# Performance work log

Hardware: AMD Instinct MI355X
Metric: run time of the kernel (lower is better)

## Reference

```python
import jax, jax.numpy as jnp
import numpy as np

NUM_CLASSES = 7
CLASS_WEIGHT = 1.0
BOX_WEIGHT = 1.0


def _linear_sum_assignment(cost):
    """Exact Hungarian via shortest augmenting paths (Jonker-Volgenant style).
    Matches scipy.optimize.linear_sum_assignment for rectangular matrices:
    returns (row_ind, col_ind) of length min(n, m), row_ind sorted ascending."""
    C = np.asarray(cost, dtype=np.float64)
    transposed = C.shape[0] > C.shape[1]
    if transposed:
        C = C.T
    n, m = C.shape  # n <= m
    u = np.zeros(n + 1)
    v = np.zeros(m + 1)
    p = np.zeros(m + 1, dtype=np.int64)    # p[j]: row matched to col j (1-based); 0 = free
    way = np.zeros(m + 1, dtype=np.int64)
    for i in range(1, n + 1):
        p[0] = i
        j0 = 0
        minv = np.full(m + 1, np.inf)
        used = np.zeros(m + 1, dtype=bool)
        while True:
            used[j0] = True
            i0 = p[j0]
            cur = C[i0 - 1] - u[i0] - v[1:]
            free = ~used[1:]
            better = free & (cur < minv[1:])
            minv[1:][better] = cur[better]
            way[1:][better] = j0
            masked = np.where(free, minv[1:], np.inf)
            j0n = int(np.argmin(masked)) + 1
            delta = masked[j0n - 1]
            uj = np.nonzero(used)[0]
            u[p[uj]] += delta
            v[uj] -= delta
            minv[1:][free] -= delta
            j0 = j0n
            if p[j0] == 0:
                break
        while j0 != 0:   # augment along alternating path
            j1 = way[j0]
            p[j0] = p[j1]
            j0 = j1
    cols = np.nonzero(p[1:] > 0)[0]
    rows = p[1:][cols] - 1
    if transposed:
        rows, cols = cols, rows
    order = np.argsort(rows)
    return rows[order], cols[order]


def _cost_matrices(pred_logits, pred_boxes, gt_labels, gt_boxes):
    """Batched cost: class_weight * (-log_softmax gathered at gt labels) + box_weight * L1 cdist on xyz."""
    B, Q, _ = pred_logits.shape
    M = gt_labels.shape[1]
    log_probs = jax.nn.log_softmax(pred_logits, axis=-1)                       # (B,Q,C)
    idx = jnp.broadcast_to(gt_labels[:, None, :], (B, Q, M))
    class_cost = -jnp.take_along_axis(log_probs, idx, axis=2)                  # (B,Q,M)
    box_cost = jnp.sum(jnp.abs(pred_boxes[:, :, None, :3] - gt_boxes[:, None, :, :3]), axis=-1)  # (B,Q,M)
    return CLASS_WEIGHT * class_cost + BOX_WEIGHT * box_cost


def _matched_loss(pred_logits, pred_boxes, gt_labels, gt_boxes, rows, cols):
    B = pred_logits.shape[0]
    bidx = jnp.arange(B)[:, None]
    ml = pred_logits[bidx, rows]          # (B,M,C) matched logits
    mb = pred_boxes[bidx, rows]           # (B,M,7) matched boxes
    gl = gt_labels[bidx, cols]            # (B,M)
    gb = gt_boxes[bidx, cols]             # (B,M,7)
    logp = jax.nn.log_softmax(ml, axis=-1)
    ce = -jnp.mean(jnp.take_along_axis(logp, gl[..., None], axis=-1)[..., 0], axis=1)  # (B,)
    l1 = jnp.mean(jnp.abs(mb - gb), axis=(1, 2))                                       # (B,)
    return jnp.mean(CLASS_WEIGHT * ce + BOX_WEIGHT * l1)


def setup_inputs() -> dict:
    key = jax.random.key(0)
    k1, k2, k3, k4 = jax.random.split(key, 4)
    B, Q, M = 128, 900, 100
    return {
        'pred_logits': jax.random.normal(k1, (B, Q, NUM_CLASSES), dtype=jnp.float32),
        'pred_boxes': jax.random.normal(k2, (B, Q, 7), dtype=jnp.float32),
        'gt_labels': jax.random.randint(k3, (B, M), 0, NUM_CLASSES, dtype=jnp.int32),
        'gt_boxes': jax.random.normal(k4, (B, M, 7), dtype=jnp.float32),
    }


def reference(pred_logits, pred_boxes, gt_labels, gt_boxes):
    B = pred_logits.shape[0]
    M = gt_labels.shape[1]
    # Assignment is done on detached costs (host-side), matching the original module.
    cost = np.asarray(_cost_matrices(pred_logits, pred_boxes, gt_labels, gt_boxes))
    rows = np.zeros((B, M), dtype=np.int64)
    cols = np.zeros((B, M), dtype=np.int64)
    for b in range(B):
        r, c = _linear_sum_assignment(cost[b])
        rows[b], cols[b] = r, c
    return _matched_loss(pred_logits, pred_boxes, gt_labels, gt_boxes,
                         jnp.asarray(rows), jnp.asarray(cols))
```

## Files before the change

### kernel.cpp

```cpp
#include <hip/hip_runtime.h>
#include <math.h>


#define NQ   900
#define NG   100
#define NC   7
#define CPL  15
#define ROUNDS 10
#define INFF __builtin_inff()

__device__ __forceinline__ float readlane_f(float x, int l) {
  return __int_as_float(__builtin_amdgcn_readlane(__float_as_int(x), l));
}

template<int CTRL>
__device__ __forceinline__ void dpp_amin_step(float &v, int &ix) {
  float v2 = __int_as_float(__builtin_amdgcn_update_dpp(
      __float_as_int(v), __float_as_int(v), CTRL, 0xf, 0xf, false));
  int i2 = __builtin_amdgcn_update_dpp(ix, ix, CTRL, 0xf, 0xf, false);
  ix = (v2 < v) ? i2 : ix;
  v  = fminf(v, v2);
}
__device__ __forceinline__ void wave_amin_b(float v, int ix, float &ov, int &oi) {
  dpp_amin_step<0x111>(v, ix);
  dpp_amin_step<0x112>(v, ix);
  dpp_amin_step<0x114>(v, ix);
  dpp_amin_step<0x118>(v, ix);
  dpp_amin_step<0x142>(v, ix);
  dpp_amin_step<0x143>(v, ix);
  ov = readlane_f(v, 63);
  oi = __builtin_amdgcn_readlane(ix, 63);
}

template<int CTRL>
__device__ __forceinline__ void dpp_amin2_step(float &a, int &ia, float &b, int &ib) {
  const int INFI = 0x7f800000;
  float a2 = __int_as_float(__builtin_amdgcn_update_dpp(
      INFI, __float_as_int(a), CTRL, 0xf, 0xf, false));
  float b2 = __int_as_float(__builtin_amdgcn_update_dpp(
      INFI, __float_as_int(b), CTRL, 0xf, 0xf, false));
  int ia2 = __builtin_amdgcn_update_dpp(0, ia, CTRL, 0xf, 0xf, false);
  int ib2 = __builtin_amdgcn_update_dpp(0, ib, CTRL, 0xf, 0xf, false);
  bool sw = a2 < a;
  float hi = sw ? a  : a2;  int ihi = sw ? ia  : ia2;
  float lo = sw ? a2 : a;   int ilo = sw ? ia2 : ia;
  bool t1 = b2 < b;
  float bb = t1 ? b2 : b;   int ibb = t1 ? ib2 : ib;
  bool t2 = hi < bb;
  b = t2 ? hi : bb;         ib = t2 ? ihi : ibb;
  a = lo; ia = ilo;
}
__device__ __forceinline__ void wave_amin2_b(float a, int ia, float b, int ib,
    float &o1, int &oc1, float &o2, int &oc2) {
  dpp_amin2_step<0x111>(a, ia, b, ib);
  dpp_amin2_step<0x112>(a, ia, b, ib);
  dpp_amin2_step<0x114>(a, ia, b, ib);
  dpp_amin2_step<0x118>(a, ia, b, ib);
  dpp_amin2_step<0x142>(a, ia, b, ib);
  dpp_amin2_step<0x143>(a, ia, b, ib);
  o1 = readlane_f(a, 63); oc1 = __builtin_amdgcn_readlane(ia, 63);
  o2 = readlane_f(b, 63); oc2 = __builtin_amdgcn_readlane(ib, 63);
}

template<int CTRL>
__device__ __forceinline__ float dpp_add_step(float x) {
  int y = __builtin_amdgcn_update_dpp(0, __float_as_int(x),
                                      CTRL, 0xf, 0xf, true);
  return x + __int_as_float(y);
}
__device__ __forceinline__ float wave_sum_b(float x) {
  x = dpp_add_step<0x111>(x);
  x = dpp_add_step<0x112>(x);
  x = dpp_add_step<0x114>(x);
  x = dpp_add_step<0x118>(x);
  x = dpp_add_step<0x142>(x);
  x = dpp_add_step<0x143>(x);
  return __int_as_float(__builtin_amdgcn_readlane(__float_as_int(x), 63));
}
__device__ __forceinline__ void gl_lds16(const float* g, float* lds_base) {
  __builtin_amdgcn_global_load_lds(
      (const __attribute__((address_space(1))) unsigned int*)g,
      (__attribute__((address_space(3))) unsigned int*)lds_base, 16, 0, 0);
}
__device__ __forceinline__ float sel7v(float a0,float a1,float a2,float a3,
                                       float a4,float a5,float a6,int lab){
  float r = a0;
  r = lab==1 ? a1 : r;  r = lab==2 ? a2 : r;  r = lab==3 ? a3 : r;
  r = lab==4 ? a4 : r;  r = lab==5 ? a5 : r;  r = lab==6 ? a6 : r;
  return r;
}

__global__ __launch_bounds__(256, 1) void hungarian_fused_kernel(
    const float* __restrict__ logits, const float* __restrict__ pboxes,
    const int* __restrict__ glabels, const float* __restrict__ gboxes,
    float* __restrict__ out, float inv_B)
{
  const int b = blockIdx.x, tid = threadIdx.x;
  const int lane = tid & 63, w = tid >> 6;

  __shared__ __align__(16) float s_raw[NQ * NC];
  __shared__ __align__(16) float s_nlpT[NC * 1024];
  __shared__ __align__(16) float s_pb[960 * NC];
  __shared__ __align__(16) float s_gb[NG * NC];
  __shared__ __align__(16) int   s_glab[NG];
  __shared__ float s_u[NG + 1];
  __shared__ float s_v[CPL * 64];
  __shared__ int   s_p[NQ];
  __shared__ unsigned s_bid[NQ];
  __shared__ int   s_rmatch[NG];
  __shared__ float s_bm1[NG], s_bm2[NG];
  __shared__ int   s_bc[NG];
  __shared__ unsigned long long s_fm[2];
  __shared__ float s_f1v[NG]; __shared__ int s_f1c[NG];
  __shared__ float s_f2v[NG]; __shared__ int s_f2c[NG];
  __shared__ int   s_mlist[128];

  {
    const float* Lg = logits + (size_t)b * NQ * NC;
    const float* Pg = pboxes + (size_t)b * NQ * NC;
    const float* Gg = gboxes + (size_t)b * NG * NC;
    const int*   Bg = glabels + (size_t)b * NG;
    #pragma unroll
    for (int t = 0; t < 7; t++) {
      int i = (t << 8) + tid;
      if (i < (NQ * NC) / 4) {
        gl_lds16(Lg + i * 4, s_raw + ((t << 8) + (w << 6)) * 4);
        gl_lds16(Pg + i * 4, s_pb  + ((t << 8) + (w << 6)) * 4);
      }
    }
    if (tid < (NG * NC) / 4) gl_lds16(Gg + tid * 4, s_gb + (w << 6) * 4);
    if (tid < NG / 4) gl_lds16((const float*)Bg + tid * 4, (float*)s_glab);
    for (int i = tid; i < (960 - NQ) * NC; i += 256) s_pb[NQ * NC + i] = 0.f;
    for (int c = tid; c < NQ; c += 256) { s_p[c] = 0x7fffffff; s_bid[c] = 0xFFFFFFFFu; }
    for (int i = tid; i < CPL * 64; i += 256) s_v[i] = 0.f;
    if (tid == 0) s_u[0] = 0.f;
  }
  __syncthreads();

  for (int i = tid; i < 960; i += 256) {
    int L = i & 63, t = i >> 6;
    int q = L * CPL + t;
    float o[NC];
    if (q < NQ) {
      float x[NC];
      #pragma unroll
      for (int c = 0; c < NC; c++) x[c] = s_raw[q * NC + c];
      float mx = x[0];
      #pragma unroll
      for (int c = 1; c < NC; c++) mx = fmaxf(mx, x[c]);
      float tt[NC]; float se = 0.f;
      #pragma unroll
      for (int c = 0; c < NC; c++) { tt[c] = x[c] - mx; se += __expf(tt[c]); }
      float lg = __logf(se);
      #pragma unroll
      for (int c = 0; c < NC; c++) o[c] = lg - tt[c];
    } else {
      #pragma unroll
      for (int c = 0; c < NC; c++) o[c] = INFF;
    }
    #pragma unroll
    for (int c = 0; c < NC; c++) s_nlpT[c * 1024 + t * 64 + L] = o[c];
  }
  __syncthreads();

  const bool lval = (lane < NQ / CPL);
  float cpx[CPL], cpy[CPL], cpz[CPL];
  #pragma unroll
  for (int t = 0; t < CPL; t++) {
    int c = lane * CPL + t;
    cpx[t]=s_pb[c*NC+0]; cpy[t]=s_pb[c*NC+1]; cpz[t]=s_pb[c*NC+2];
  }

  for (int rl = 0; rl < 25; rl++) {
    int r = w * 25 + rl;
    int lab = s_glab[r];
    float gx = s_gb[r*NC+0], gy = s_gb[r*NC+1], gz = s_gb[r*NC+2];
    float m1 = INFF; int c1t = 0;
    #pragma unroll
    for (int t = 0; t < CPL; t++) {
      float nl = s_nlpT[lab*1024 + t*64 + lane];
      float bs = fabsf(cpx[t]-gx)+fabsf(cpy[t]-gy)+fabsf(cpz[t]-gz);
      float cost = nl + bs;
      bool lt1 = cost < m1;
      c1t = lt1 ? t : c1t;
      m1 = fminf(m1, cost);
    }
    float w1; int col;
    wave_amin_b(m1, lane * CPL + c1t, w1, col);
    if (lane == 0) {
      s_u[r + 1] = w1;
      s_bc[r] = col;
      atomicMin(&s_p[col], r + 1);
    }
  }
  __syncthreads();
  for (int c = tid; c < NQ; c += 256) if (s_p[c] == 0x7fffffff) s_p[c] = 0;
  if (tid < NG) {
    int c = s_bc[tid];
    s_rmatch[tid] = (s_p[c] == tid + 1) ? c + 1 : 0;
  }
  __syncthreads();

  for (int round = 0; round < ROUNDS; round++) {
    if (w == 0) {
      unsigned long long m = __ballot(s_rmatch[lane] == 0);
      if (lane == 0) s_fm[0] = m;
    } else if (w == 1) {
      unsigned long long m = __ballot((lane < NG - 64) && s_rmatch[64 + lane] == 0);
      if (lane == 0) s_fm[1] = m;
    }
    __syncthreads();
    const unsigned long long fm0r = s_fm[0], fm1r = s_fm[1];
    if ((fm0r | fm1r) == 0) break;
    float vreg[CPL];
    #pragma unroll
    for (int t = 0; t < CPL; t++) vreg[t] = s_v[t*64 + lane];
    {
      unsigned long long mm0 = fm0r, mm1 = fm1r;
      int idx = 0;
      while (mm0 | mm1) {
        int r;
        if (mm0) { int b2 = (int)__builtin_ctzll(mm0); mm0 &= mm0 - 1; r = b2; }
        else     { int b2 = (int)__builtin_ctzll(mm1); mm1 &= mm1 - 1; r = 64 + b2; }
        if ((idx++ & 3) != w) continue;
        int lab = s_glab[r];
        float gx = s_gb[r*NC+0], gy = s_gb[r*NC+1], gz = s_gb[r*NC+2];
        float m1 = INFF, m2 = INFF; int c1t = 0;
        #pragma unroll
        for (int t = 0; t < CPL; t++) {
          float nl = s_nlpT[lab*1024 + t*64 + lane];
          float bs = fabsf(cpx[t]-gx)+fabsf(cpy[t]-gy)+fabsf(cpz[t]-gz);
          float cost = (nl + bs) - vreg[t];
          bool lt1 = cost < m1;
          m2 = lt1 ? m1 : fminf(m2, cost);
          c1t = lt1 ? t : c1t;
          m1 = fminf(m1, cost);
        }
        float w1, w2; int col1, dumc;
        wave_amin2_b(m1, lane * CPL + c1t, m2, 0, w1, col1, w2, dumc);
        if (lane == 0) {
          s_bm1[r] = w1; s_bm2[r] = w2; s_bc[r] = col1;
          atomicMin(&s_bid[col1],
                    (__float_as_uint(w1) & 0xFFFFFF80u) | (unsigned)(r + 1));
        }
      }
    }
    __syncthreads();
    if (tid < NG) {
      bool wasfree = (tid < 64) ? ((fm0r >> tid) & 1ull)
                                : ((fm1r >> (tid - 64)) & 1ull);
      if (wasfree) {
        int c = s_bc[tid];
        if ((s_bid[c] & 0x7Fu) == (unsigned)(tid + 1)) {
          int dold = s_p[c];
          s_p[c] = tid + 1;
          s_rmatch[tid] = c + 1;
          if (dold > 0) s_rmatch[dold - 1] = 0;
          s_u[tid + 1] = s_bm2[tid];
          s_v[(c % CPL) * 64 + (c / CPL)] -= (s_bm2[tid] - s_bm1[tid]);
        }
      }
    }
    __syncthreads();
    if (tid < NG) {
      bool wasfree = (tid < 64) ? ((fm0r >> tid) & 1ull)
                                : ((fm1r >> (tid - 64)) & 1ull);
      if (wasfree) s_bid[s_bc[tid]] = 0xFFFFFFFFu;
    }
  }
  __syncthreads();

  if (w == 0) {
    unsigned long long m = __ballot(s_rmatch[lane] == 0);
    if (lane == 0) s_fm[0] = m;
  } else if (w == 1) {
    unsigned long long m = __ballot((lane < NG - 64) && s_rmatch[64 + lane] == 0);
    if (lane == 0) s_fm[1] = m;
  }
  __syncthreads();
  const unsigned long long ff0 = s_fm[0], ff1 = s_fm[1];
  const int nfinal = __popcll(ff0) + __popcll(ff1);

  if (nfinal > 0) {
    float vreg[CPL];
    #pragma unroll
    for (int t = 0; t < CPL; t++) vreg[t] = s_v[t*64 + lane];
    unsigned long long mm0 = ff0, mm1 = ff1;
    int idx = 0;
    while (mm0 | mm1) {
      int r;
      if (mm0) { int b2 = (int)__builtin_ctzll(mm0); mm0 &= mm0 - 1; r = b2; }
      else     { int b2 = (int)__builtin_ctzll(mm1); mm1 &= mm1 - 1; r = 64 + b2; }
      if ((idx++ & 3) != w) continue;
      int lab = s_glab[r];
      float gx = s_gb[r*NC+0], gy = s_gb[r*NC+1], gz = s_gb[r*NC+2];
      float m1 = INFF; int c1t = 0;
      #pragma unroll
      for (int t = 0; t < CPL; t++) {
        float nl = s_nlpT[lab*1024 + t*64 + lane];
        float bs = fabsf(cpx[t]-gx)+fabsf(cpy[t]-gy)+fabsf(cpz[t]-gz);
        float cost = (nl + bs) - vreg[t];
        bool lt1 = cost < m1;
        c1t = lt1 ? t : c1t;
        m1 = fminf(m1, cost);
      }
      float w1; int col;
      wave_amin_b(m1, lane * CPL + c1t, w1, col);
      if (lane == 0) { s_u[r + 1] = w1; s_bc[r] = col; }
    }
    __syncthreads();
    if (tid < NG) {
      bool wasfree = (tid < 64) ? ((ff0 >> tid) & 1ull)
                                : ((ff1 >> (tid - 64)) & 1ull);
      if (wasfree) {
        int c = s_bc[tid];
        if (s_p[c] == 0) atomicMin(&s_bid[c], (unsigned)tid);
      }
    }
    __syncthreads();
    if (tid < NG) {
      bool wasfree = (tid < 64) ? ((ff0 >> tid) & 1ull)
                                : ((ff1 >> (tid - 64)) & 1ull);
      if (wasfree) {
        int c = s_bc[tid];
        if (s_p[c] == 0 && s_bid[c] == (unsigned)tid) {
          s_p[c] = tid + 1;
          s_rmatch[tid] = c + 1;
        }
      }
    }
    __syncthreads();
    if (w == 0) {
      unsigned long long m = __ballot(s_rmatch[lane] == 0);
      if (lane == 0) s_fm[0] = m;
    } else if (w == 1) {
      unsigned long long m = __ballot((lane < NG - 64) && s_rmatch[64 + lane] == 0);
      if (lane == 0) s_fm[1] = m;
    }
    __syncthreads();
  }

  const unsigned long long gg0 = s_fm[0], gg1 = s_fm[1];
  const int nf2 = __popcll(gg0) + __popcll(gg1);

  if (nf2 > 0) {
  unsigned fmask = 0;
  if (lval) {
    #pragma unroll
    for (int t = 0; t < CPL; t++)
      if (s_p[lane * CPL + t] == 0) fmask |= (1u << t);
  }

  auto top2row = [&](int lab, float gx, float gy, float gz,
                     float &o1v, int &o1c, float &o2v, int &o2c) {
    float m1 = INFF, m2 = INFF; int c1 = 0, c2 = 0;
    #pragma unroll
    for (int t = 0; t < CPL; t++) {
      float nl = s_nlpT[lab*1024 + t*64 + lane];
      float bs = fabsf(cpx[t]-gx)+fabsf(cpy[t]-gy)+fabsf(cpz[t]-gz);
      float cost = nl + bs;
      cost = ((fmask >> t) & 1u) ? cost : INFF;
      bool lt1 = cost < m1;
      bool lt2 = cost < m2;
      c2 = lt1 ? c1 : (lt2 ? t : c2);
      m2 = lt1 ? m1 : fminf(m2, cost);
      c1 = lt1 ? t : c1;
      m1 = fminf(m1, cost);
    }
    wave_amin2_b(m1, lane * CPL + c1, m2, lane * CPL + c2, o1v, o1c, o2v, o2c);
  };

  for (int rl = 0; rl < 25; rl++) {
    int r = w * 25 + rl;
    int lab = s_glab[r];
    float gx = s_gb[r*NC+0], gy = s_gb[r*NC+1], gz = s_gb[r*NC+2];
    float v1, v2; int cc1, cc2;
    top2row(lab, gx, gy, gz, v1, cc1, v2, cc2);
    if (lane == 0) {
      s_f1v[r] = v1; s_f1c[r] = cc1; s_f2v[r] = v2; s_f2c[r] = cc2;
    }
  }
  __syncthreads();
  if (w != 0) return;

  volatile float* vu = s_u;

  const bool r1ok = (lane < NG - 64);
  int   rlab0 = s_glab[lane];
  float rgx0 = s_gb[lane*NC+0], rgy0 = s_gb[lane*NC+1], rgz0 = s_gb[lane*NC+2];
  int   rlab1 = 0; float rgx1=0.f, rgy1=0.f, rgz1=0.f;
  if (r1ok) {
    int r = 64 + lane;
    rlab1 = s_glab[r];
    rgx1 = s_gb[r*NC+0]; rgy1 = s_gb[r*NC+1]; rgz1 = s_gb[r*NC+2];
  }
  float ru0 = vu[lane + 1];
  float ru1 = r1ok ? vu[lane + 65] : 0.f;
  float rf1v0 = s_f1v[lane];       int rf1c0 = s_f1c[lane];
  float rf2v0 = s_f2v[lane];       int rf2c0 = s_f2c[lane];
  float rf1v1 = r1ok ? s_f1v[64+lane] : INFF; int rf1c1 = r1ok ? s_f1c[64+lane] : -1;
  float rf2v1 = r1ok ? s_f2v[64+lane] : INFF; int rf2c1 = r1ok ? s_f2c[64+lane] : -1;

  unsigned long long fm0 = gg0;
  unsigned long long fm1 = gg1;

  int NM = 0;
  #pragma unroll
  for (int t = 0; t < CPL; t++) {
    int c = lane * CPL + t;
    bool has = lval && (s_p[c] > 0);
    unsigned long long m = __ballot(has);
    int pos = NM + (int)__popcll(m & ((1ull << lane) - 1ull));
    if (has) s_mlist[pos] = c;
    NM += (int)__popcll(m);
  }

  int   mcol[2]  = {-1,-1};
  int   mprow[2] = {0,0};
  float mpu[2]   = {0.f,0.f};
  float mv[2]    = {0.f,0.f};
  float mx[2]={0,0}, my[2]={0,0}, mz[2]={0,0};
  float mn0[2],mn1[2],mn2[2],mn3[2],mn4[2],mn5[2],mn6[2];
  #pragma unroll
  for (int k = 0; k < 2; k++) { mn0[k]=0;mn1[k]=0;mn2[k]=0;mn3[k]=0;mn4[k]=0;mn5[k]=0;mn6[k]=0; }
  #pragma unroll
  for (int k = 0; k < 2; k++) {
    int s = lane + (k << 6);
    if (s < NM) {
      int c = s_mlist[s];
      int cq = c / CPL, ct = c - cq * CPL;
      mcol[k] = c;
      mx[k] = s_pb[c*NC+0]; my[k] = s_pb[c*NC+1]; mz[k] = s_pb[c*NC+2];
      mn0[k] = s_nlpT[0*1024 + ct*64 + cq];
      mn1[k] = s_nlpT[1*1024 + ct*64 + cq];
      mn2[k] = s_nlpT[2*1024 + ct*64 + cq];
      mn3[k] = s_nlpT[3*1024 + ct*64 + cq];
      mn4[k] = s_nlpT[4*1024 + ct*64 + cq];
      mn5[k] = s_nlpT[5*1024 + ct*64 + cq];
      mn6[k] = s_nlpT[6*1024 + ct*64 + cq];
      mprow[k] = s_p[c];
      mpu[k] = vu[mprow[k]];
      mv[k] = s_v[ct * 64 + cq];
    }
  }

  float dsl[2]; int wsl[2];

  for (int half = 0; half < 2; half++) {
    unsigned long long fm = half ? fm1 : fm0;
    while (fm) {
      int bit = (int)__builtin_ctzll(fm);
      fm &= fm - 1;
      int rfree = bit + (half ? 65 : 1);
      dsl[0] = INFF; dsl[1] = INFF; wsl[0] = 0; wsl[1] = 0;
      unsigned usedm = 0;
      float bfv = INFF; int bfc = -1, bfprev = 0;
      int i0 = rfree;
      int ro0 = rfree - 1;
      float u_i0 = readlane_f((ro0 >> 6) ? ru1 : ru0, ro0 & 63);
      int j0p = 0;
      float minVal = 0.f;
      int jf = -1, jfprev = 0;

      for (int it = 0; it < 128; it++) {
        int ro = i0 - 1, rown = ro & 63, rs = ro >> 6;
        int   lab = __builtin_amdgcn_readlane(rs ? rlab1 : rlab0, rown);
        float gx = readlane_f(rs ? rgx1 : rgx0, rown);
        float gy = readlane_f(rs ? rgy1 : rgy0, rown);
        float gz = readlane_f(rs ? rgz1 : rgz0, rown);
        float hs = minVal - u_i0;
        float f1v = readlane_f(rs ? rf1v1 : rf1v0, rown);
        int   f1c = __builtin_amdgcn_readlane(rs ? rf1c1 : rf1c0, rown);
        float cbf = f1v + hs;
        if (cbf < bfv) { bfv = cbf; bfc = f1c; bfprev = j0p; }
        float lb = INFF; int bk = 0;
        #pragma unroll
        for (int k = 0; k < 2; k++) {
          bool gate = ((lane + (k << 6)) < NM) && !((usedm >> k) & 1u);
          float nl = sel7v(mn0[k],mn1[k],mn2[k],mn3[k],mn4[k],mn5[k],mn6[k],lab);
          float bs = fabsf(mx[k]-gx)+fabsf(my[k]-gy)+fabsf(mz[k]-gz);
          float rr = ((nl + bs) + hs) - mv[k];
          bool imp = gate && (rr < dsl[k]);
          dsl[k] = imp ? rr : dsl[k];
          wsl[k] = imp ? j0p : wsl[k];
          float cand = gate ? dsl[k] : INFF;
          bool bt = cand < lb;
          bk = bt ? k : bk;
          lb = fminf(lb, cand);
        }
        float dm; int spk;
        wave_amin_b(lb, (bk << 6) | lane, dm, spk);
        if (bfv <= dm) { minVal = bfv; jf = bfc; jfprev = bfprev; break; }
        minVal = dm;
        int so = spk & 63, sk = spk >> 6;
        usedm |= (lane == so) ? (1u << sk) : 0u;
        i0  = __builtin_amdgcn_readlane(sk ? mprow[1] : mprow[0], so);
        u_i0 = readlane_f(sk ? mpu[1] : mpu[0], so);
        j0p = spk + 1;
      }
      if (jf < 0) { jf = bfc; jfprev = bfprev; minVal = bfv; }

      if (lane == 0) vu[rfree] += minVal;
      #pragma unroll
      for (int k = 0; k < 2; k++) {
        if ((usedm >> k) & 1u) {
          float a = minVal - dsl[k];
          mv[k] -= a;
          vu[mprow[k]] += a;
        }
      }
      __threadfence_block();

      int pred = jfprev;
      int nr;
      if (pred == 0) nr = rfree;
      else {
        int s = pred - 1;
        nr = __builtin_amdgcn_readlane((s >> 6) ? mprow[1] : mprow[0], s & 63);
      }
      if (lane == 0) s_p[jf] = nr;
      {
        int cq = jf / CPL, ct = jf - cq * CPL;
        float nx = s_pb[jf*NC+0], ny = s_pb[jf*NC+1], nz = s_pb[jf*NC+2];
        float a0 = s_nlpT[0*1024 + ct*64 + cq];
        float a1 = s_nlpT[1*1024 + ct*64 + cq];
        float a2 = s_nlpT[2*1024 + ct*64 + cq];
        float a3 = s_nlpT[3*1024 + ct*64 + cq];
        float a4 = s_nlpT[4*1024 + ct*64 + cq];
        float a5 = s_nlpT[5*1024 + ct*64 + cq];
        float a6 = s_nlpT[6*1024 + ct*64 + cq];
        int kk = NM >> 6;
        if (lane == (NM & 63) && NM < 128) {
          if (kk == 0) {
            mcol[0]=jf; mx[0]=nx; my[0]=ny; mz[0]=nz; mprow[0]=nr; mv[0]=0.f;
            mn0[0]=a0;mn1[0]=a1;mn2[0]=a2;mn3[0]=a3;mn4[0]=a4;mn5[0]=a5;mn6[0]=a6;
          } else {
            mcol[1]=jf; mx[1]=nx; my[1]=ny; mz[1]=nz; mprow[1]=nr; mv[1]=0.f;
            mn0[1]=a0;mn1[1]=a1;mn2[1]=a2;mn3[1]=a3;mn4[1]=a4;mn5[1]=a5;mn6[1]=a6;
          }
        }
        NM++;
      }
      while (pred) {
        int s = pred - 1, so = s & 63, sk = s >> 6;
        int np = __builtin_amdgcn_readlane(sk ? wsl[1] : wsl[0], so);
        int nr2;
        if (np == 0) nr2 = rfree;
        else {
          int s2 = np - 1;
          nr2 = __builtin_amdgcn_readlane((s2 >> 6) ? mprow[1] : mprow[0], s2 & 63);
        }
        int sc = __builtin_amdgcn_readlane(sk ? mcol[1] : mcol[0], so);
        if (lane == so) { if (sk) mprow[1] = nr2; else mprow[0] = nr2; }
        if (lane == 0) s_p[sc] = nr2;
        pred = np;
      }
      __threadfence_block();

      ru0 = vu[lane + 1];
      if (r1ok) ru1 = vu[lane + 65];
      #pragma unroll
      for (int k = 0; k < 2; k++)
        if ((lane + (k << 6)) < NM) mpu[k] = vu[mprow[k]];

      if (lane == (jf / CPL)) fmask &= ~(1u << (jf - (jf / CPL) * CPL));
      if (rf1c0 == jf) { rf1v0 = rf2v0; rf1c0 = rf2c0; rf2c0 = -1; rf2v0 = INFF; }
      else if (rf2c0 == jf) { rf2c0 = -1; rf2v0 = INFF; }
      if (rf1c1 == jf) { rf1v1 = rf2v1; rf1c1 = rf2c1; rf2c1 = -1; rf2v1 = INFF; }
      else if (rf2c1 == jf) { rf2c1 = -1; rf2v1 = INFF; }
      unsigned long long need0 = __ballot(rf1c0 < 0);
      unsigned long long need1 = __ballot(r1ok && (rf1c1 < 0));
      while (need0) {
        int rb = (int)__builtin_ctzll(need0); need0 &= need0 - 1;
        int lab = __builtin_amdgcn_readlane(rlab0, rb);
        float gx = readlane_f(rgx0, rb), gy = readlane_f(rgy0, rb), gz = readlane_f(rgz0, rb);
        float v1, v2; int cc1, cc2;
        top2row(lab, gx, gy, gz, v1, cc1, v2, cc2);
        if (lane == rb) { rf1v0=v1; rf1c0=cc1; rf2v0=v2; rf2c0=cc2; }
      }
      while (need1) {
        int rb = (int)__builtin_ctzll(need1); need1 &= need1 - 1;
        int lab = __builtin_amdgcn_readlane(rlab1, rb);
        float gx = readlane_f(rgx1, rb), gy = readlane_f(rgy1, rb), gz = readlane_f(rgz1, rb);
        float v1, v2; int cc1, cc2;
        top2row(lab, gx, gy, gz, v1, cc1, v2, cc2);
        if (lane == rb) { rf1v1=v1; rf1c1=cc1; rf2v1=v2; rf2c1=cc2; }
      }
    }
  }
  }

  if (w != 0) return;
  {
    float ce = 0.f, l1 = 0.f;
    if (lval) {
      #pragma unroll
      for (int t = 0; t < CPL; t++) {
        int c = lane * CPL + t;
        int pr = s_p[c];
        if (pr > 0) {
          int g = pr - 1;
          int lg = s_glab[g];
          ce += s_nlpT[lg*1024 + t*64 + lane];
          float s = 0.f;
          #pragma unroll
          for (int d7 = 0; d7 < 7; d7++) s += fabsf(s_pb[c*NC+d7] - s_gb[g*NC+d7]);
          l1 += s;
        }
      }
    }
    float tot = ce * (1.f / NG) + l1 * (1.f / (NG * 7.f));
    tot = wave_sum_b(tot);
    if (lane == 0) atomicAdd(out, tot * inv_B);
  }
}

extern "C" void kernel_launch(void* const* d_in, const int* in_sizes, int n_in,
                              void* d_out, int out_size, void* d_ws, size_t ws_size,
                              hipStream_t stream) {
  const float* logits  = (const float*)d_in[0];
  const float* pboxes  = (const float*)d_in[1];
  const int*   glabels = (const int*)d_in[2];
  const float* gboxes  = (const float*)d_in[3];
  float* out = (float*)d_out;
  const int B = in_sizes[0] / (NQ * NC);

  hungarian_fused_kernel<<<dim3(B), dim3(256), 0, stream>>>(
      logits, pboxes, glabels, gboxes, out, 1.0f / (float)B);
}
```

Measured before the change: 129.3 us.

## Adaptive auction rounds with stall exit and top-4 free-column cache per row

The fixed 10-round parallel auction loop becomes adaptive. It runs at least 10 and at most 24 rounds, and exits early once the free-row count stops dropping for 3 rounds. The per-row cache of cheapest free columns grows from 2 to 4 entries, so the serial augmenting phase recomputes a full row scan less often when cached columns get taken. The cost is a second reduction pass per row refill, more registers and LDS, and possibly extra auction rounds that may not shorten the serial phase.

```diff
diff --git a/kernel.cpp b/kernel.cpp
--- a/kernel.cpp
+++ b/kernel.cpp
@@ -6,7 +6,8 @@
 #define NG   100
 #define NC   7
 #define CPL  15
-#define ROUNDS 10
+#define MAXROUNDS 24
+#define MINROUNDS 10
 #define INFF __builtin_inff()
 
 __device__ __forceinline__ float readlane_f(float x, int l) {
@@ -89,6 +90,13 @@
   r = lab==4 ? a4 : r;  r = lab==5 ? a5 : r;  r = lab==6 ? a6 : r;
   return r;
 }
+__device__ __forceinline__ void list_drop(int jf,
+    float &v0,int &c0, float &v1,int &c1, float &v2,int &c2, float &v3,int &c3) {
+  if      (c0 == jf) { v0=v1;c0=c1; v1=v2;c1=c2; v2=v3;c2=c3; v3=INFF;c3=-1; }
+  else if (c1 == jf) {              v1=v2;c1=c2; v2=v3;c2=c3; v3=INFF;c3=-1; }
+  else if (c2 == jf) {                           v2=v3;c2=c3; v3=INFF;c3=-1; }
+  else if (c3 == jf) {                                        v3=INFF;c3=-1; }
+}
 
 __global__ __launch_bounds__(256, 1) void hungarian_fused_kernel(
     const float* __restrict__ logits, const float* __restrict__ pboxes,
@@ -111,8 +119,7 @@
   __shared__ float s_bm1[NG], s_bm2[NG];
   __shared__ int   s_bc[NG];
   __shared__ unsigned long long s_fm[2];
-  __shared__ float s_f1v[NG]; __shared__ int s_f1c[NG];
-  __shared__ float s_f2v[NG]; __shared__ int s_f2c[NG];
+  __shared__ float s_fv[4][NG]; __shared__ int s_fc[4][NG];
   __shared__ int   s_mlist[128];
 
   {
@@ -201,71 +208,77 @@
   }
   __syncthreads();
 
-  for (int round = 0; round < ROUNDS; round++) {
-    if (w == 0) {
-      unsigned long long m = __ballot(s_rmatch[lane] == 0);
-      if (lane == 0) s_fm[0] = m;
-    } else if (w == 1) {
-      unsigned long long m = __ballot((lane < NG - 64) && s_rmatch[64 + lane] == 0);
-      if (lane == 0) s_fm[1] = m;
-    }
-    __syncthreads();
-    const unsigned long long fm0r = s_fm[0], fm1r = s_fm[1];
-    if ((fm0r | fm1r) == 0) break;
-    float vreg[CPL];
-    #pragma unroll
-    for (int t = 0; t < CPL; t++) vreg[t] = s_v[t*64 + lane];
-    {
-      unsigned long long mm0 = fm0r, mm1 = fm1r;
-      int idx = 0;
-      while (mm0 | mm1) {
-        int r;
-        if (mm0) { int b2 = (int)__builtin_ctzll(mm0); mm0 &= mm0 - 1; r = b2; }
-        else     { int b2 = (int)__builtin_ctzll(mm1); mm1 &= mm1 - 1; r = 64 + b2; }
-        if ((idx++ & 3) != w) continue;
-        int lab = s_glab[r];
-        float gx = s_gb[r*NC+0], gy = s_gb[r*NC+1], gz = s_gb[r*NC+2];
-        float m1 = INFF, m2 = INFF; int c1t = 0;
-        #pragma unroll
-        for (int t = 0; t < CPL; t++) {
-          float nl = s_nlpT[lab*1024 + t*64 + lane];
-          float bs = fabsf(cpx[t]-gx)+fabsf(cpy[t]-gy)+fabsf(cpz[t]-gz);
-          float cost = (nl + bs) - vreg[t];
-          bool lt1 = cost < m1;
-          m2 = lt1 ? m1 : fminf(m2, cost);
-          c1t = lt1 ? t : c1t;
-          m1 = fminf(m1, cost);
-        }
-        float w1, w2; int col1, dumc;
-        wave_amin2_b(m1, lane * CPL + c1t, m2, 0, w1, col1, w2, dumc);
-        if (lane == 0) {
-          s_bm1[r] = w1; s_bm2[r] = w2; s_bc[r] = col1;
-          atomicMin(&s_bid[col1],
-                    (__float_as_uint(w1) & 0xFFFFFF80u) | (unsigned)(r + 1));
-        }
-      }
-    }
-    __syncthreads();
-    if (tid < NG) {
-      bool wasfree = (tid < 64) ? ((fm0r >> tid) & 1ull)
-                                : ((fm1r >> (tid - 64)) & 1ull);
-      if (wasfree) {
-        int c = s_bc[tid];
-        if ((s_bid[c] & 0x7Fu) == (unsigned)(tid + 1)) {
-          int dold = s_p[c];
-          s_p[c] = tid + 1;
-          s_rmatch[tid] = c + 1;
-          if (dold > 0) s_rmatch[dold - 1] = 0;
-          s_u[tid + 1] = s_bm2[tid];
-          s_v[(c % CPL) * 64 + (c / CPL)] -= (s_bm2[tid] - s_bm1[tid]);
-        }
-      }
-    }
-    __syncthreads();
-    if (tid < NG) {
-      bool wasfree = (tid < 64) ? ((fm0r >> tid) & 1ull)
-                                : ((fm1r >> (tid - 64)) & 1ull);
-      if (wasfree) s_bid[s_bc[tid]] = 0xFFFFFFFFu;
+  {
+    int bestFree = 0x7fffffff, stall = 0;
+    for (int round = 0; round < MAXROUNDS; round++) {
+      if (w == 0) {
+        unsigned long long m = __ballot(s_rmatch[lane] == 0);
+        if (lane == 0) s_fm[0] = m;
+      } else if (w == 1) {
+        unsigned long long m = __ballot((lane < NG - 64) && s_rmatch[64 + lane] == 0);
+        if (lane == 0) s_fm[1] = m;
+      }
+      __syncthreads();
+      const unsigned long long fm0r = s_fm[0], fm1r = s_fm[1];
+      int nfree = __popcll(fm0r) + __popcll(fm1r);
+      if (nfree == 0) break;
+      if (nfree < bestFree) { bestFree = nfree; stall = 0; } else stall++;
+      if (round >= MINROUNDS && stall >= 3) break;
+      float vreg[CPL];
+      #pragma unroll
+      for (int t = 0; t < CPL; t++) vreg[t] = s_v[t*64 + lane];
+      {
+        unsigned long long mm0 = fm0r, mm1 = fm1r;
+        int idx = 0;
+        while (mm0 | mm1) {
+          int r;
+          if (mm0) { int b2 = (int)__builtin_ctzll(mm0); mm0 &= mm0 - 1; r = b2; }
+          else     { int b2 = (int)__builtin_ctzll(mm1); mm1 &= mm1 - 1; r = 64 + b2; }
+          if ((idx++ & 3) != w) continue;
+          int lab = s_glab[r];
+          float gx = s_gb[r*NC+0], gy = s_gb[r*NC+1], gz = s_gb[r*NC+2];
+          float m1 = INFF, m2 = INFF; int c1t = 0;
+          #pragma unroll
+          for (int t = 0; t < CPL; t++) {
+            float nl = s_nlpT[lab*1024 + t*64 + lane];
+            float bs = fabsf(cpx[t]-gx)+fabsf(cpy[t]-gy)+fabsf(cpz[t]-gz);
+            float cost = (nl + bs) - vreg[t];
+            bool lt1 = cost < m1;
+            m2 = lt1 ? m1 : fminf(m2, cost);
+            c1t = lt1 ? t : c1t;
+            m1 = fminf(m1, cost);
+          }
+          float w1, w2; int col1, dumc;
+          wave_amin2_b(m1, lane * CPL + c1t, m2, 0, w1, col1, w2, dumc);
+          if (lane == 0) {
+            s_bm1[r] = w1; s_bm2[r] = w2; s_bc[r] = col1;
+            atomicMin(&s_bid[col1],
+                      (__float_as_uint(w1) & 0xFFFFFF80u) | (unsigned)(r + 1));
+          }
+        }
+      }
+      __syncthreads();
+      if (tid < NG) {
+        bool wasfree = (tid < 64) ? ((fm0r >> tid) & 1ull)
+                                  : ((fm1r >> (tid - 64)) & 1ull);
+        if (wasfree) {
+          int c = s_bc[tid];
+          if ((s_bid[c] & 0x7Fu) == (unsigned)(tid + 1)) {
+            int dold = s_p[c];
+            s_p[c] = tid + 1;
+            s_rmatch[tid] = c + 1;
+            if (dold > 0) s_rmatch[dold - 1] = 0;
+            s_u[tid + 1] = s_bm2[tid];
+            s_v[(c % CPL) * 64 + (c / CPL)] -= (s_bm2[tid] - s_bm1[tid]);
+          }
+        }
+      }
+      __syncthreads();
+      if (tid < NG) {
+        bool wasfree = (tid < 64) ? ((fm0r >> tid) & 1ull)
+                                  : ((fm1r >> (tid - 64)) & 1ull);
+        if (wasfree) s_bid[s_bc[tid]] = 0xFFFFFFFFu;
+      }
     }
   }
   __syncthreads();
@@ -351,8 +364,9 @@
       if (s_p[lane * CPL + t] == 0) fmask |= (1u << t);
   }
 
-  auto top2row = [&](int lab, float gx, float gy, float gz,
-                     float &o1v, int &o1c, float &o2v, int &o2c) {
+  auto top4row = [&](int lab, float gx, float gy, float gz,
+                     float &o1v, int &o1c, float &o2v, int &o2c,
+                     float &o3v, int &o3c, float &o4v, int &o4c) {
     float m1 = INFF, m2 = INFF; int c1 = 0, c2 = 0;
     #pragma unroll
     for (int t = 0; t < CPL; t++) {
@@ -368,16 +382,36 @@
       m1 = fminf(m1, cost);
     }
     wave_amin2_b(m1, lane * CPL + c1, m2, lane * CPL + c2, o1v, o1c, o2v, o2c);
+    float n1 = INFF, n2 = INFF; int d1 = 0, d2 = 0;
+    #pragma unroll
+    for (int t = 0; t < CPL; t++) {
+      int myc = lane * CPL + t;
+      float nl = s_nlpT[lab*1024 + t*64 + lane];
+      float bs = fabsf(cpx[t]-gx)+fabsf(cpy[t]-gy)+fabsf(cpz[t]-gz);
+      float cost = nl + bs;
+      bool ok = ((fmask >> t) & 1u) && (myc != o1c) && (myc != o2c);
+      cost = ok ? cost : INFF;
+      bool lt1 = cost < n1;
+      bool lt2 = cost < n2;
+      d2 = lt1 ? d1 : (lt2 ? t : d2);
+      n2 = lt1 ? n1 : fminf(n2, cost);
+      d1 = lt1 ? t : d1;
+      n1 = fminf(n1, cost);
+    }
+    wave_amin2_b(n1, lane * CPL + d1, n2, lane * CPL + d2, o3v, o3c, o4v, o4c);
   };
 
   for (int rl = 0; rl < 25; rl++) {
     int r = w * 25 + rl;
     int lab = s_glab[r];
     float gx = s_gb[r*NC+0], gy = s_gb[r*NC+1], gz = s_gb[r*NC+2];
-    float v1, v2; int cc1, cc2;
-    top2row(lab, gx, gy, gz, v1, cc1, v2, cc2);
+    float v1, v2, v3, v4; int cc1, cc2, cc3, cc4;
+    top4row(lab, gx, gy, gz, v1, cc1, v2, cc2, v3, cc3, v4, cc4);
     if (lane == 0) {
-      s_f1v[r] = v1; s_f1c[r] = cc1; s_f2v[r] = v2; s_f2c[r] = cc2;
+      s_fv[0][r] = v1; s_fc[0][r] = cc1;
+      s_fv[1][r] = v2; s_fc[1][r] = cc2;
+      s_fv[2][r] = v3; s_fc[2][r] = cc3;
+      s_fv[3][r] = v4; s_fc[3][r] = cc4;
     }
   }
   __syncthreads();
@@ -396,10 +430,12 @@
   }
   float ru0 = vu[lane + 1];
   float ru1 = r1ok ? vu[lane + 65] : 0.f;
-  float rf1v0 = s_f1v[lane];       int rf1c0 = s_f1c[lane];
-  float rf2v0 = s_f2v[lane];       int rf2c0 = s_f2c[lane];
-  float rf1v1 = r1ok ? s_f1v[64+lane] : INFF; int rf1c1 = r1ok ? s_f1c[64+lane] : -1;
-  float rf2v1 = r1ok ? s_f2v[64+lane] : INFF; int rf2c1 = r1ok ? s_f2c[64+lane] : -1;
+  float aV0 = s_fv[0][lane], aV1 = s_fv[1][lane], aV2 = s_fv[2][lane], aV3 = s_fv[3][lane];
+  int   aC0 = s_fc[0][lane], aC1 = s_fc[1][lane], aC2 = s_fc[2][lane], aC3 = s_fc[3][lane];
+  float bV0 = r1ok ? s_fv[0][64+lane] : INFF, bV1 = r1ok ? s_fv[1][64+lane] : INFF;
+  float bV2 = r1ok ? s_fv[2][64+lane] : INFF, bV3 = r1ok ? s_fv[3][64+lane] : INFF;
+  int   bC0 = r1ok ? s_fc[0][64+lane] : -1,   bC1 = r1ok ? s_fc[1][64+lane] : -1;
+  int   bC2 = r1ok ? s_fc[2][64+lane] : -1,   bC3 = r1ok ? s_fc[3][64+lane] : -1;
 
   unsigned long long fm0 = gg0;
   unsigned long long fm1 = gg1;
@@ -469,8 +505,8 @@
         float gy = readlane_f(rs ? rgy1 : rgy0, rown);
         float gz = readlane_f(rs ? rgz1 : rgz0, rown);
         float hs = minVal - u_i0;
-        float f1v = readlane_f(rs ? rf1v1 : rf1v0, rown);
-        int   f1c = __builtin_amdgcn_readlane(rs ? rf1c1 : rf1c0, rown);
+        float f1v = readlane_f(rs ? bV0 : aV0, rown);
+        int   f1c = __builtin_amdgcn_readlane(rs ? bC0 : aC0, rown);
         float cbf = f1v + hs;
         if (cbf < bfv) { bfv = cbf; bfc = f1c; bfprev = j0p; }
         float lb = INFF; int bk = 0;
@@ -564,27 +600,25 @@
         if ((lane + (k << 6)) < NM) mpu[k] = vu[mprow[k]];
 
       if (lane == (jf / CPL)) fmask &= ~(1u << (jf - (jf / CPL) * CPL));
-      if (rf1c0 == jf) { rf1v0 = rf2v0; rf1c0 = rf2c0; rf2c0 = -1; rf2v0 = INFF; }
-      else if (rf2c0 == jf) { rf2c0 = -1; rf2v0 = INFF; }
-      if (rf1c1 == jf) { rf1v1 = rf2v1; rf1c1 = rf2c1; rf2c1 = -1; rf2v1 = INFF; }
-      else if (rf2c1 == jf) { rf2c1 = -1; rf2v1 = INFF; }
-      unsigned long long need0 = __ballot(rf1c0 < 0);
-      unsigned long long need1 = __ballot(r1ok && (rf1c1 < 0));
+      list_drop(jf, aV0,aC0, aV1,aC1, aV2,aC2, aV3,aC3);
+      list_drop(jf, bV0,bC0, bV1,bC1, bV2,bC2, bV3,bC3);
+      unsigned long long need0 = __ballot(aC0 < 0);
+      unsigned long long need1 = __ballot(r1ok && (bC0 < 0));
       while (need0) {
         int rb = (int)__builtin_ctzll(need0); need0 &= need0 - 1;
         int lab = __builtin_amdgcn_readlane(rlab0, rb);
         float gx = readlane_f(rgx0, rb), gy = readlane_f(rgy0, rb), gz = readlane_f(rgz0, rb);
-        float v1, v2; int cc1, cc2;
-        top2row(lab, gx, gy, gz, v1, cc1, v2, cc2);
-        if (lane == rb) { rf1v0=v1; rf1c0=cc1; rf2v0=v2; rf2c0=cc2; }
+        float v1, v2, v3, v4; int cc1, cc2, cc3, cc4;
+        top4row(lab, gx, gy, gz, v1, cc1, v2, cc2, v3, cc3, v4, cc4);
+        if (lane == rb) { aV0=v1;aC0=cc1; aV1=v2;aC1=cc2; aV2=v3;aC2=cc3; aV3=v4;aC3=cc4; }
       }
       while (need1) {
         int rb = (int)__builtin_ctzll(need1); need1 &= need1 - 1;
         int lab = __builtin_amdgcn_readlane(rlab1, rb);
         float gx = readlane_f(rgx1, rb), gy = readlane_f(rgy1, rb), gz = readlane_f(rgz1, rb);
-        float v1, v2; int cc1, cc2;
-        top2row(lab, gx, gy, gz, v1, cc1, v2, cc2);
-        if (lane == rb) { rf1v1=v1; rf1c1=cc1; rf2v1=v2; rf2c1=cc2; }
+        float v1, v2, v3, v4; int cc1, cc2, cc3, cc4;
+        top4row(lab, gx, gy, gz, v1, cc1, v2, cc2, v3, cc3, v4, cc4);
+        if (lane == rb) { bV0=v1;bC0=cc1; bV1=v2;bC1=cc2; bV2=v3;bC2=cc3; bV3=v4;bC3=cc4; }
       }
     }
   }
```

Result: slower. 149.8 us (+15.9%).
